# Optimization experiments

Hardware: AMD Instinct MI355X
Metric: run time of the kernel (lower is better)

## Reference

```python
import jax, jax.numpy as jnp
import numpy as np

N_GENE = 4762
N_CELL = 847


def _graph_conv(x_src, src, dst, n_src, n_dst, W, b):
    """DGL GraphConv with norm='both': D_src^{-1/2} A D_dst^{-1/2} X W + b."""
    ones_e = jnp.ones(src.shape, jnp.float32)
    deg_out = jax.ops.segment_sum(ones_e, src, num_segments=n_src)
    norm_src = jnp.clip(deg_out, 1.0, None) ** -0.5
    feat = x_src * norm_src[:, None]            # [n_src, d]
    msg = feat[src]                              # gather  [E, d]
    agg = jax.ops.segment_sum(msg, dst, num_segments=n_dst)  # scatter-add [n_dst, d]
    deg_in = jax.ops.segment_sum(ones_e, dst, num_segments=n_dst)
    norm_dst = jnp.clip(deg_in, 1.0, None) ** -0.5
    return (agg * norm_dst[:, None]) @ W + b


def setup_inputs() -> dict:
    key = jax.random.key(0)
    ks = jax.random.split(key, 12)
    E = 200000
    d = 256
    inp = {
        "gene_emb": jax.random.normal(ks[0], (N_GENE, d), jnp.float32),
        "cell_emb": jax.random.normal(ks[1], (N_CELL, d), jnp.float32),
        "W_g2c": jax.random.normal(ks[2], (d, d), jnp.float32) * (1.0 / np.sqrt(d)),
        "b_g2c": jnp.zeros((d,), jnp.float32),
        "W_c2g": jax.random.normal(ks[3], (d, d), jnp.float32) * (1.0 / np.sqrt(d)),
        "b_c2g": jnp.zeros((d,), jnp.float32),
        "Wp": jax.random.normal(ks[4], (2 * d, 1), jnp.float32) * (1.0 / np.sqrt(2 * d)),
        "bp": jnp.zeros((1,), jnp.float32),
        "g2c_src": jax.random.randint(ks[5], (E,), 0, N_GENE, jnp.int32),
        "g2c_dst": jax.random.randint(ks[6], (E,), 0, N_CELL, jnp.int32),
        "c2g_src": jax.random.randint(ks[7], (E,), 0, N_CELL, jnp.int32),
        "c2g_dst": jax.random.randint(ks[8], (E,), 0, N_GENE, jnp.int32),
        "dec_src": jax.random.randint(ks[9], (E,), 0, N_GENE, jnp.int32),
        "dec_dst": jax.random.randint(ks[10], (E,), 0, N_CELL, jnp.int32),
    }
    return inp


def reference(gene_emb, cell_emb, W_g2c, b_g2c, W_c2g, b_c2g, Wp, bp,
              g2c_src, g2c_dst, c2g_src, c2g_dst, dec_src, dec_dst):
    # HeteroGraphConv (aggregate='sum'): each dst type receives from one relation here.
    h_cell = _graph_conv(gene_emb, g2c_src, g2c_dst, N_GENE, N_CELL, W_g2c, b_g2c)
    h_gene = _graph_conv(cell_emb, c2g_src, c2g_dst, N_CELL, N_GENE, W_c2g, b_c2g)
    h_gene = jax.nn.relu(h_gene)
    h_cell = jax.nn.relu(h_cell)
    # HeteroMLPPredictor: concat(src_h, dst_h) @ Wp + bp on dec_graph edges.
    x = jnp.concatenate([h_gene[dec_src], h_cell[dec_dst]], axis=1)  # [E_dec, 512]
    score = x @ Wp + bp                                               # [E_dec, 1]
    return (score, h_gene, h_cell)
```

## Files before the change

kernel.cpp:

```cpp
#include <hip/hip_runtime.h>

#define N_GENE 4762
#define N_CELL 847
#define NEDGE  200000
#define D      256
#define NPART  64

typedef __attribute__((ext_vector_type(8))) short short8;
typedef __attribute__((ext_vector_type(8))) unsigned short ushort8v;
typedef __attribute__((ext_vector_type(4))) float f32x4;

#define S_G_OUT 0
#define S_C_IN  (S_G_OUT + N_GENE)
#define S_C_OUT (S_C_IN + N_CELL)
#define S_G_IN  (S_C_OUT + N_CELL)
#define NBINS   (S_G_IN + N_GENE)

#define ALIGN8(x) (((x) + 7) & ~7)

#define A_DEG      0
#define A_NRM      (A_DEG + NBINS)
#define A_OFFS_C   (A_NRM + NBINS)
#define A_OFFS_G   (A_OFFS_C + N_CELL + 1)
#define A_SORT_C   ALIGN8(A_OFFS_G + N_GENE + 1)
#define A_SORT_G   (A_SORT_C + 2 * NEDGE)
#define A_PART     (A_SORT_G + 2 * NEDGE)
#define A_SG       (A_PART + NPART * NBINS)
#define A_SC       (A_SG + N_GENE)
#define A_GENE_BF  ALIGN8(A_SC + N_CELL)
#define A_CELL_BF  ALIGN8(A_GENE_BF + N_GENE * D / 2)
#define A_WT1_BF   ALIGN8(A_CELL_BF + N_CELL * D / 2)
#define A_WT2_BF   ALIGN8(A_WT1_BF + D * D / 2)
#define A_AGGC_BF  ALIGN8(A_WT2_BF + D * D / 2)
#define A_AGGG_BF  ALIGN8(A_AGGC_BF + N_CELL * D / 2)

__device__ __forceinline__ unsigned short f2bf(float f) {
    unsigned u = __float_as_uint(f);
    u = (u + 0x7FFFu + ((u >> 16) & 1u)) >> 16;
    return (unsigned short)u;
}
__device__ __forceinline__ float bf2f(unsigned short b) {
    return __uint_as_float(((unsigned)b) << 16);
}

__global__ __launch_bounds__(1024) void k_pre(
        const int* __restrict__ g2c_src, const int* __restrict__ g2c_dst,
        const int* __restrict__ c2g_src, const int* __restrict__ c2g_dst,
        const float* __restrict__ gene_emb, const float* __restrict__ cell_emb,
        const float* __restrict__ W_g2c, const float* __restrict__ W_c2g,
        int* __restrict__ partial,
        unsigned short* __restrict__ gene_bf, unsigned short* __restrict__ cell_bf,
        unsigned short* __restrict__ wt1, unsigned short* __restrict__ wt2) {
    __shared__ int sh[NBINS];
    int B = blockIdx.x, T = threadIdx.x;
    if (B < NPART) {
        for (int j = T; j < NBINS; j += 1024) sh[j] = 0;
        __syncthreads();
        const int chunk = (NEDGE + NPART - 1) / NPART;
        int e0 = B * chunk, e1 = min(NEDGE, e0 + chunk);
        for (int e = e0 + T; e < e1; e += 1024) {
            atomicAdd(&sh[S_G_OUT + g2c_src[e]], 1);
            atomicAdd(&sh[S_C_IN  + g2c_dst[e]], 1);
            atomicAdd(&sh[S_C_OUT + c2g_src[e]], 1);
            atomicAdd(&sh[S_G_IN  + c2g_dst[e]], 1);
        }
        __syncthreads();
        int* pp = partial + B * NBINS;
        for (int j = T; j < NBINS; j += 1024) pp[j] = sh[j];
    } else {
        const int NG = N_GENE * D, NC = N_CELL * D, NW = D * D;
        const int total = NG + NC + 2 * NW;
        for (int i = (B - NPART) * 1024 + T; i < total; i += NPART * 1024) {
            if (i < NG) {
                gene_bf[i] = f2bf(gene_emb[i]);
            } else if (i < NG + NC) {
                int j = i - NG;
                cell_bf[j] = f2bf(cell_emb[j]);
            } else if (i < NG + NC + NW) {
                int j = i - NG - NC;
                wt1[j] = f2bf(W_g2c[(j & 255) * D + (j >> 8)]);
            } else {
                int j = i - NG - NC - NW;
                wt2[j] = f2bf(W_c2g[(j & 255) * D + (j >> 8)]);
            }
        }
    }
}

__global__ void k_reduce(int* __restrict__ partial, int* __restrict__ deg,
                         float* __restrict__ nrm) {
    int j = blockIdx.x * blockDim.x + threadIdx.x;
    if (j < NBINS) {
        int s = 0;
        #pragma unroll
        for (int b0 = 0; b0 < NPART; b0 += 32) {
            int t[32];
            #pragma unroll
            for (int u = 0; u < 32; u++) t[u] = partial[(b0 + u) * NBINS + j];
            #pragma unroll
            for (int u = 0; u < 32; u++) { partial[(b0 + u) * NBINS + j] = s; s += t[u]; }
        }
        deg[j] = s;
        nrm[j] = rsqrtf(fmaxf((float)s, 1.0f));
    }
}

__global__ __launch_bounds__(1024) void k_scatter(
        const int* __restrict__ g2c_src, const int* __restrict__ g2c_dst,
        const int* __restrict__ c2g_src, const int* __restrict__ c2g_dst,
        const int* __restrict__ deg, const int* __restrict__ partial,
        const float* __restrict__ nrm,
        int* __restrict__ offsC, int* __restrict__ offsG,
        int2* __restrict__ sortC, int2* __restrict__ sortG) {
    __shared__ int soffs[N_GENE + 1];
    __shared__ int scur[N_GENE];
    __shared__ int wsum[16];
    int T = threadIdx.x, blk = blockIdx.x, dir = blockIdx.y;
    const int* src  = dir ? c2g_src : g2c_src;
    const int* dst  = dir ? c2g_dst : g2c_dst;
    const int* dgs  = dir ? deg + S_G_IN : deg + S_C_IN;
    const float* nsv = dir ? nrm + S_C_OUT : nrm + S_G_OUT;
    int seg         = dir ? S_G_IN : S_C_IN;
    int nb          = dir ? N_GENE : N_CELL;
    int* goffs      = dir ? offsG : offsC;
    int2* sorted    = dir ? sortG : sortC;
    int per = (nb + 1023) >> 10;
    int i0 = T * per, i1 = min(nb, i0 + per);
    int loc[5];
    int s = 0;
    for (int i = i0; i < i1; i++) { loc[i - i0] = s; s += dgs[i]; }
    int lane = T & 63, w = T >> 6;
    int t = s;
    #pragma unroll
    for (int off = 1; off < 64; off <<= 1) {
        int u = __shfl_up(t, off);
        if (lane >= off) t += u;
    }
    if (lane == 63) wsum[w] = t;
    __syncthreads();
    if (w == 0 && lane < 16) {
        int x = wsum[lane];
        #pragma unroll
        for (int off = 1; off < 16; off <<= 1) {
            int u = __shfl_up(x, off);
            if (lane >= off) x += u;
        }
        wsum[lane] = x;
    }
    __syncthreads();
    int wbase = w ? wsum[w - 1] : 0;
    int excl = wbase + t - s;
    for (int i = i0; i < i1; i++) soffs[i] = excl + loc[i - i0];
    if (T == 1023) soffs[nb] = excl + s;
    __syncthreads();
    if (blk == 0)
        for (int j = T; j <= nb; j += 1024) goffs[j] = soffs[j];
    const int* basep = partial + blk * NBINS + seg;
    for (int j = T; j < nb; j += 1024) scur[j] = soffs[j] + basep[j];
    __syncthreads();
    const int chunk = (NEDGE + NPART - 1) / NPART;
    int e0 = blk * chunk, e1 = min(NEDGE, e0 + chunk);
    for (int e = e0 + T; e < e1; e += 1024) {
        int d = dst[e], sv = src[e];
        float nv = nsv[sv];
        int pos = atomicAdd(&scur[d], 1);
        sorted[pos] = make_int2(sv, __float_as_int(nv));
    }
}

__global__ __launch_bounds__(256) void k_agg(
        const unsigned short* __restrict__ gene_bf,
        const unsigned short* __restrict__ cell_bf,
        const int2* __restrict__ sortC, const int2* __restrict__ sortG,
        const int* __restrict__ offsC, const int* __restrict__ offsG,
        const float* __restrict__ nrm,
        unsigned short* __restrict__ aggC, unsigned short* __restrict__ aggG) {
    __shared__ int   sidx[4][64];
    __shared__ float snrm[4][64];
    __shared__ float pacc[4][256];
    int w = threadIdx.x >> 6, lane = threadIdx.x & 63;
    int half = lane >> 5, li = lane & 31;
    int B = blockIdx.x;
    bool isCell = B < N_CELL;

    int e0, e1;
    const unsigned short* emb;
    const int2* sorted;
    int node;
    if (isCell) {
        node = B;
        int f0 = offsC[node], f1 = offsC[node + 1];
        int ne = f1 - f0, nw = (ne + 3) >> 2;
        e0 = f0 + w * nw; e1 = min(f1, e0 + nw);
        emb = gene_bf; sorted = sortC;
    } else {
        node = (B - N_CELL) * 4 + w;
        if (node >= N_GENE) return;
        e0 = offsG[node]; e1 = offsG[node + 1];
        emb = cell_bf; sorted = sortG;
    }

    float acc[8];
    #pragma unroll
    for (int c = 0; c < 8; c++) acc[c] = 0.f;

    for (int base = e0; base < e1; base += 64) {
        int n = min(64, e1 - base);
        if (lane < n) {
            int2 pr = sorted[base + lane];
            sidx[w][lane] = pr.x;
            snrm[w][lane] = __int_as_float(pr.y);
        }
        int i = 0;
        for (; 2 * i + 8 <= n; i += 4) {
            int j0 = 2 * i + half, j1 = 2 * i + 2 + half;
            int j2 = 2 * i + 4 + half, j3 = 2 * i + 6 + half;
            ushort8v v0 = *(const ushort8v*)&emb[sidx[w][j0] * D + li * 8];
            ushort8v v1 = *(const ushort8v*)&emb[sidx[w][j1] * D + li * 8];
            ushort8v v2 = *(const ushort8v*)&emb[sidx[w][j2] * D + li * 8];
            ushort8v v3 = *(const ushort8v*)&emb[sidx[w][j3] * D + li * 8];
            float n0 = snrm[w][j0], n1 = snrm[w][j1];
            float n2 = snrm[w][j2], n3 = snrm[w][j3];
            #pragma unroll
            for (int c = 0; c < 8; c++)
                acc[c] += bf2f(v0[c]) * n0 + bf2f(v1[c]) * n1 +
                          bf2f(v2[c]) * n2 + bf2f(v3[c]) * n3;
        }
        int npair = (n + 1) >> 1;
        for (; i < npair; i++) {
            int jj = 2 * i + half;
            bool ok = jj < n;
            int idx = ok ? sidx[w][jj] : sidx[w][0];
            float nv = ok ? snrm[w][jj] : 0.f;
            ushort8v v = *(const ushort8v*)&emb[idx * D + li * 8];
            #pragma unroll
            for (int c = 0; c < 8; c++) acc[c] += bf2f(v[c]) * nv;
        }
    }
    #pragma unroll
    for (int c = 0; c < 8; c++) acc[c] += __shfl_xor(acc[c], 32);

    if (isCell) {
        if (half == 0) {
            #pragma unroll
            for (int c = 0; c < 8; c++) pacc[w][li * 8 + c] = acc[c];
        }
        __syncthreads();
        int T = threadIdx.x;
        float s2 = pacc[0][T] + pacc[1][T] + pacc[2][T] + pacc[3][T];
        aggC[node * D + T] = f2bf(s2 * nrm[S_C_IN + node]);
    } else {
        if (half == 0) {
            float ndv = nrm[S_G_IN + node];
            ushort8v o;
            #pragma unroll
            for (int c = 0; c < 8; c++) o[c] = f2bf(acc[c] * ndv);
            *(ushort8v*)&aggG[node * D + li * 8] = o;
        }
    }
}

__global__ __launch_bounds__(256) void k_gemm2(
        const unsigned short* __restrict__ aggC, const unsigned short* __restrict__ aggG,
        const unsigned short* __restrict__ wt1, const unsigned short* __restrict__ wt2,
        const float* __restrict__ b_g2c, const float* __restrict__ b_c2g,
        const float* __restrict__ Wp,
        float* __restrict__ hC, float* __restrict__ hG,
        float* __restrict__ sg, float* __restrict__ sc) {
    const int CT = (N_CELL + 15) / 16;
    const int GT = (N_GENE + 15) / 16;
    int wid = blockIdx.x * 4 + (threadIdx.x >> 6);
    if (wid >= CT + GT) return;
    bool isCell = wid < CT;
    int tile = isCell ? wid : wid - CT;
    int m0 = tile * 16;
    int M = isCell ? N_CELL : N_GENE;
    const unsigned short* A  = isCell ? aggC : aggG;
    const unsigned short* Wt = isCell ? wt1 : wt2;
    const float* bias = isCell ? b_g2c : b_c2g;
    const float* wp   = isCell ? Wp + D : Wp;
    float* H  = isCell ? hC : hG;
    float* sv = isCell ? sc : sg;
    int lane = threadIdx.x & 63;
    int l15 = lane & 15, quad = lane >> 4;
    int arow = m0 + l15;
    if (arow >= M) arow = M - 1;
    f32x4 acc[16];
    #pragma unroll
    for (int t = 0; t < 16; t++) acc[t] = (f32x4){0.f, 0.f, 0.f, 0.f};
    #pragma unroll
    for (int k0 = 0; k0 < D; k0 += 32) {
        short8 a = *(const short8*)&A[arow * D + k0 + quad * 8];
        #pragma unroll
        for (int t = 0; t < 16; t++) {
            short8 b = *(const short8*)&Wt[(t * 16 + l15) * D + k0 + quad * 8];
            acc[t] = __builtin_amdgcn_mfma_f32_16x16x32_bf16(a, b, acc[t], 0, 0, 0);
        }
    }
    float dot[4] = {0.f, 0.f, 0.f, 0.f};
    #pragma unroll
    for (int t = 0; t < 16; t++) {
        int col = t * 16 + l15;
        float bv = bias[col], wv = wp[col];
        #pragma unroll
        for (int r = 0; r < 4; r++) {
            int row = m0 + quad * 4 + r;
            float h = fmaxf(acc[t][r] + bv, 0.f);
            if (row < M) H[row * D + col] = h;
            dot[r] += h * wv;
        }
    }
    #pragma unroll
    for (int off = 1; off < 16; off <<= 1) {
        #pragma unroll
        for (int r = 0; r < 4; r++) dot[r] += __shfl_xor(dot[r], off);
    }
    if (l15 == 0) {
        #pragma unroll
        for (int r = 0; r < 4; r++) {
            int row = m0 + quad * 4 + r;
            if (row < M) sv[row] = dot[r];
        }
    }
}

__global__ void k_score(const int* __restrict__ dsrc, const int* __restrict__ ddst,
                        const float* __restrict__ sg, const float* __restrict__ sc,
                        const float* __restrict__ bp, float* __restrict__ out) {
    int i = blockIdx.x * blockDim.x + threadIdx.x;
    if (i < NEDGE) out[i] = sg[dsrc[i]] + sc[ddst[i]] + bp[0];
}

extern "C" void kernel_launch(void* const* d_in, const int* in_sizes, int n_in,
                              void* d_out, int out_size, void* d_ws, size_t ws_size,
                              hipStream_t stream) {
    const float* gene_emb = (const float*)d_in[0];
    const float* cell_emb = (const float*)d_in[1];
    const float* W_g2c    = (const float*)d_in[2];
    const float* b_g2c    = (const float*)d_in[3];
    const float* W_c2g    = (const float*)d_in[4];
    const float* b_c2g    = (const float*)d_in[5];
    const float* Wp       = (const float*)d_in[6];
    const float* bp       = (const float*)d_in[7];
    const int* g2c_src = (const int*)d_in[8];
    const int* g2c_dst = (const int*)d_in[9];
    const int* c2g_src = (const int*)d_in[10];
    const int* c2g_dst = (const int*)d_in[11];
    const int* dec_src = (const int*)d_in[12];
    const int* dec_dst = (const int*)d_in[13];

    int*   wsi = (int*)d_ws;
    float* wsf = (float*)d_ws;
    unsigned short* gene_bf = (unsigned short*)(wsi + A_GENE_BF);
    unsigned short* cell_bf = (unsigned short*)(wsi + A_CELL_BF);
    unsigned short* wt1     = (unsigned short*)(wsi + A_WT1_BF);
    unsigned short* wt2     = (unsigned short*)(wsi + A_WT2_BF);
    unsigned short* aggC    = (unsigned short*)(wsi + A_AGGC_BF);
    unsigned short* aggG    = (unsigned short*)(wsi + A_AGGG_BF);
    int2* sortC = (int2*)(wsi + A_SORT_C);
    int2* sortG = (int2*)(wsi + A_SORT_G);

    float* out = (float*)d_out;
    float* out_score = out;
    float* out_hgene = out + NEDGE;
    float* out_hcell = out + NEDGE + N_GENE * D;

    k_pre<<<2 * NPART, 1024, 0, stream>>>(g2c_src, g2c_dst, c2g_src, c2g_dst,
                                          gene_emb, cell_emb, W_g2c, W_c2g,
                                          wsi + A_PART, gene_bf, cell_bf, wt1, wt2);
    k_reduce<<<(NBINS + 255) / 256, 256, 0, stream>>>(wsi + A_PART, wsi + A_DEG,
                                                      wsf + A_NRM);
    {
        dim3 grid(NPART, 2);
        k_scatter<<<grid, 1024, 0, stream>>>(g2c_src, g2c_dst, c2g_src, c2g_dst,
                                             wsi + A_DEG, wsi + A_PART, wsf + A_NRM,
                                             wsi + A_OFFS_C, wsi + A_OFFS_G,
                                             sortC, sortG);
    }
    k_agg<<<N_CELL + (N_GENE + 3) / 4, 256, 0, stream>>>(
        gene_bf, cell_bf, sortC, sortG, wsi + A_OFFS_C, wsi + A_OFFS_G,
        wsf + A_NRM, aggC, aggG);
    {
        const int CT = (N_CELL + 15) / 16, GT = (N_GENE + 15) / 16;
        k_gemm2<<<(CT + GT + 3) / 4, 256, 0, stream>>>(aggC, aggG, wt1, wt2,
                                                       b_g2c, b_c2g, Wp,
                                                       out_hcell, out_hgene,
                                                       wsf + A_SG, wsf + A_SC);
    }
    k_score<<<(NEDGE + 255) / 256, 256, 0, stream>>>(dec_src, dec_dst,
                                                     wsf + A_SG, wsf + A_SC, bp, out_score);
}
```

Baseline: 158.9 us.

## Split offset scan into separate kernel, raise edge partitions, unroll gather by eight

Raises the number of edge partitions from 64 to 256 so the histogram and scatter kernels spread across more blocks. The per-block prefix scan moves into a small standalone kernel that runs once per direction, so the scatter blocks no longer repeat it. The scatter kernel also stages the source norms in shared memory instead of reading them from global memory per edge. The aggregation kernel gains an 8-way unrolled gather loop for more memory-level parallelism. In exchange there is one extra kernel launch, the partial-count buffer grows fourfold so the reduce kernel reads more data, and the larger shared-memory use may lower scatter occupancy.

```diff
diff --git a/kernel.cpp b/kernel.cpp
--- a/kernel.cpp
+++ b/kernel.cpp
@@ -4,7 +4,7 @@
 #define N_CELL 847
 #define NEDGE  200000
 #define D      256
-#define NPART  64
+#define NPART  256
 
 typedef __attribute__((ext_vector_type(8))) short short8;
 typedef __attribute__((ext_vector_type(8))) unsigned short ushort8v;
@@ -70,7 +70,7 @@
     } else {
         const int NG = N_GENE * D, NC = N_CELL * D, NW = D * D;
         const int total = NG + NC + 2 * NW;
-        for (int i = (B - NPART) * 1024 + T; i < total; i += NPART * 1024) {
+        for (int i = (B - NPART) * 1024 + T; i < total; i += 64 * 1024) {
             if (i < NG) {
                 gene_bf[i] = f2bf(gene_emb[i]);
             } else if (i < NG + NC) {
@@ -92,7 +92,6 @@
     int j = blockIdx.x * blockDim.x + threadIdx.x;
     if (j < NBINS) {
         int s = 0;
-        #pragma unroll
         for (int b0 = 0; b0 < NPART; b0 += 32) {
             int t[32];
             #pragma unroll
@@ -105,25 +104,14 @@
     }
 }
 
-__global__ __launch_bounds__(1024) void k_scatter(
-        const int* __restrict__ g2c_src, const int* __restrict__ g2c_dst,
-        const int* __restrict__ c2g_src, const int* __restrict__ c2g_dst,
-        const int* __restrict__ deg, const int* __restrict__ partial,
-        const float* __restrict__ nrm,
-        int* __restrict__ offsC, int* __restrict__ offsG,
-        int2* __restrict__ sortC, int2* __restrict__ sortG) {
-    __shared__ int soffs[N_GENE + 1];
-    __shared__ int scur[N_GENE];
+__global__ __launch_bounds__(1024) void k_scan(const int* __restrict__ deg,
+                                               int* __restrict__ offsC,
+                                               int* __restrict__ offsG) {
     __shared__ int wsum[16];
-    int T = threadIdx.x, blk = blockIdx.x, dir = blockIdx.y;
-    const int* src  = dir ? c2g_src : g2c_src;
-    const int* dst  = dir ? c2g_dst : g2c_dst;
-    const int* dgs  = dir ? deg + S_G_IN : deg + S_C_IN;
-    const float* nsv = dir ? nrm + S_C_OUT : nrm + S_G_OUT;
-    int seg         = dir ? S_G_IN : S_C_IN;
-    int nb          = dir ? N_GENE : N_CELL;
-    int* goffs      = dir ? offsG : offsC;
-    int2* sorted    = dir ? sortG : sortC;
+    int dir = blockIdx.x, T = threadIdx.x;
+    const int* dgs = dir ? deg + S_G_IN : deg + S_C_IN;
+    int nb         = dir ? N_GENE : N_CELL;
+    int* goffs     = dir ? offsG : offsC;
     int per = (nb + 1023) >> 10;
     int i0 = T * per, i1 = min(nb, i0 + per);
     int loc[5];
@@ -150,19 +138,38 @@
     __syncthreads();
     int wbase = w ? wsum[w - 1] : 0;
     int excl = wbase + t - s;
-    for (int i = i0; i < i1; i++) soffs[i] = excl + loc[i - i0];
-    if (T == 1023) soffs[nb] = excl + s;
+    for (int i = i0; i < i1; i++) goffs[i] = excl + loc[i - i0];
+    if (T == 1023) goffs[nb] = excl + s;
+}
+
+__global__ __launch_bounds__(1024) void k_scatter(
+        const int* __restrict__ g2c_src, const int* __restrict__ g2c_dst,
+        const int* __restrict__ c2g_src, const int* __restrict__ c2g_dst,
+        const int* __restrict__ partial, const float* __restrict__ nrm,
+        const int* __restrict__ offsC, const int* __restrict__ offsG,
+        int2* __restrict__ sortC, int2* __restrict__ sortG) {
+    __shared__ int   scur[N_GENE];
+    __shared__ float nsrcf[N_GENE];
+    int T = threadIdx.x, blk = blockIdx.x, dir = blockIdx.y;
+    const int* src   = dir ? c2g_src : g2c_src;
+    const int* dst   = dir ? c2g_dst : g2c_dst;
+    int seg          = dir ? S_G_IN : S_C_IN;
+    int sseg         = dir ? S_C_OUT : S_G_OUT;
+    int nb           = dir ? N_GENE : N_CELL;
+    int ns           = dir ? N_CELL : N_GENE;
+    const int* goffs = dir ? offsG : offsC;
+    int2* sorted     = dir ? sortG : sortC;
+
+    for (int j = T; j < ns; j += 1024) nsrcf[j] = nrm[sseg + j];
+    const int* basep = partial + blk * NBINS + seg;
+    for (int j = T; j < nb; j += 1024) scur[j] = goffs[j] + basep[j];
     __syncthreads();
-    if (blk == 0)
-        for (int j = T; j <= nb; j += 1024) goffs[j] = soffs[j];
-    const int* basep = partial + blk * NBINS + seg;
-    for (int j = T; j < nb; j += 1024) scur[j] = soffs[j] + basep[j];
-    __syncthreads();
+
     const int chunk = (NEDGE + NPART - 1) / NPART;
     int e0 = blk * chunk, e1 = min(NEDGE, e0 + chunk);
     for (int e = e0 + T; e < e1; e += 1024) {
         int d = dst[e], sv = src[e];
-        float nv = nsv[sv];
+        float nv = nsrcf[sv];
         int pos = atomicAdd(&scur[d], 1);
         sorted[pos] = make_int2(sv, __float_as_int(nv));
     }
@@ -212,6 +219,23 @@
             snrm[w][lane] = __int_as_float(pr.y);
         }
         int i = 0;
+        for (; 2 * i + 16 <= n; i += 8) {
+            ushort8v v[8];
+            float nv[8];
+            #pragma unroll
+            for (int k = 0; k < 8; k++) {
+                int jj = 2 * i + 2 * k + half;
+                v[k] = *(const ushort8v*)&emb[sidx[w][jj] * D + li * 8];
+                nv[k] = snrm[w][jj];
+            }
+            #pragma unroll
+            for (int c = 0; c < 8; c++) {
+                float s0 = 0.f;
+                #pragma unroll
+                for (int k = 0; k < 8; k++) s0 += bf2f(v[k][c]) * nv[k];
+                acc[c] += s0;
+            }
+        }
         for (; 2 * i + 8 <= n; i += 4) {
             int j0 = 2 * i + half, j1 = 2 * i + 2 + half;
             int j2 = 2 * i + 4 + half, j3 = 2 * i + 6 + half;
@@ -365,15 +389,16 @@
     float* out_hgene = out + NEDGE;
     float* out_hcell = out + NEDGE + N_GENE * D;
 
-    k_pre<<<2 * NPART, 1024, 0, stream>>>(g2c_src, g2c_dst, c2g_src, c2g_dst,
-                                          gene_emb, cell_emb, W_g2c, W_c2g,
-                                          wsi + A_PART, gene_bf, cell_bf, wt1, wt2);
+    k_pre<<<NPART + 64, 1024, 0, stream>>>(g2c_src, g2c_dst, c2g_src, c2g_dst,
+                                           gene_emb, cell_emb, W_g2c, W_c2g,
+                                           wsi + A_PART, gene_bf, cell_bf, wt1, wt2);
     k_reduce<<<(NBINS + 255) / 256, 256, 0, stream>>>(wsi + A_PART, wsi + A_DEG,
                                                       wsf + A_NRM);
+    k_scan<<<2, 1024, 0, stream>>>(wsi + A_DEG, wsi + A_OFFS_C, wsi + A_OFFS_G);
     {
         dim3 grid(NPART, 2);
         k_scatter<<<grid, 1024, 0, stream>>>(g2c_src, g2c_dst, c2g_src, c2g_dst,
-                                             wsi + A_DEG, wsi + A_PART, wsf + A_NRM,
+                                             wsi + A_PART, wsf + A_NRM,
                                              wsi + A_OFFS_C, wsi + A_OFFS_G,
                                              sortC, sortG);
     }
```

Result: slower. 169.9 us (+6.9%).

## Split degree histogram per index array, unroll aggregation by 8, split GEMM over N

Applied to the files above, without the earlier changes.

The degree-count kernel now gives each of the four edge index arrays its own group of 64 blocks, which uses a smaller shared histogram and adds more parallelism. The aggregation loop gains an 8-pair unrolled path so more gather loads are in flight at once. The final GEMM gives each wave a 64-column quarter of the output rather than all 256 columns, so four times as many waves are launched with fewer accumulator registers each. Because each row's score dot product is now split across waves, it is combined with float atomics into buffers zeroed in the prep kernel, which makes the summation order nondeterministic.

```diff
diff --git a/kernel.cpp b/kernel.cpp
--- a/kernel.cpp
+++ b/kernel.cpp
@@ -50,27 +50,30 @@
         const float* __restrict__ W_g2c, const float* __restrict__ W_c2g,
         int* __restrict__ partial,
         unsigned short* __restrict__ gene_bf, unsigned short* __restrict__ cell_bf,
-        unsigned short* __restrict__ wt1, unsigned short* __restrict__ wt2) {
-    __shared__ int sh[NBINS];
+        unsigned short* __restrict__ wt1, unsigned short* __restrict__ wt2,
+        float* __restrict__ sg, float* __restrict__ sc) {
+    __shared__ int sh[N_GENE];
     int B = blockIdx.x, T = threadIdx.x;
-    if (B < NPART) {
-        for (int j = T; j < NBINS; j += 1024) sh[j] = 0;
+    if (B < 4 * NPART) {
+        int grp = B >> 6, blk = B & (NPART - 1);
+        const int* idx;
+        int segbase, segn;
+        if      (grp == 0) { idx = g2c_src; segbase = S_G_OUT; segn = N_GENE; }
+        else if (grp == 1) { idx = g2c_dst; segbase = S_C_IN;  segn = N_CELL; }
+        else if (grp == 2) { idx = c2g_src; segbase = S_C_OUT; segn = N_CELL; }
+        else               { idx = c2g_dst; segbase = S_G_IN;  segn = N_GENE; }
+        for (int j = T; j < segn; j += 1024) sh[j] = 0;
         __syncthreads();
         const int chunk = (NEDGE + NPART - 1) / NPART;
-        int e0 = B * chunk, e1 = min(NEDGE, e0 + chunk);
-        for (int e = e0 + T; e < e1; e += 1024) {
-            atomicAdd(&sh[S_G_OUT + g2c_src[e]], 1);
-            atomicAdd(&sh[S_C_IN  + g2c_dst[e]], 1);
-            atomicAdd(&sh[S_C_OUT + c2g_src[e]], 1);
-            atomicAdd(&sh[S_G_IN  + c2g_dst[e]], 1);
-        }
+        int e0 = blk * chunk, e1 = min(NEDGE, e0 + chunk);
+        for (int e = e0 + T; e < e1; e += 1024) atomicAdd(&sh[idx[e]], 1);
         __syncthreads();
-        int* pp = partial + B * NBINS;
-        for (int j = T; j < NBINS; j += 1024) pp[j] = sh[j];
+        int* pp = partial + blk * NBINS + segbase;
+        for (int j = T; j < segn; j += 1024) pp[j] = sh[j];
     } else {
         const int NG = N_GENE * D, NC = N_CELL * D, NW = D * D;
         const int total = NG + NC + 2 * NW;
-        for (int i = (B - NPART) * 1024 + T; i < total; i += NPART * 1024) {
+        for (int i = (B - 4 * NPART) * 1024 + T; i < total; i += 64 * 1024) {
             if (i < NG) {
                 gene_bf[i] = f2bf(gene_emb[i]);
             } else if (i < NG + NC) {
@@ -83,6 +86,9 @@
                 int j = i - NG - NC - NW;
                 wt2[j] = f2bf(W_c2g[(j & 255) * D + (j >> 8)]);
             }
+        }
+        for (int i = (B - 4 * NPART) * 1024 + T; i < N_GENE + N_CELL; i += 64 * 1024) {
+            if (i < N_GENE) sg[i] = 0.f; else sc[i - N_GENE] = 0.f;
         }
     }
 }
@@ -212,6 +218,23 @@
             snrm[w][lane] = __int_as_float(pr.y);
         }
         int i = 0;
+        for (; 2 * i + 16 <= n; i += 8) {
+            ushort8v v[8];
+            float nv[8];
+            #pragma unroll
+            for (int k = 0; k < 8; k++) {
+                int jj = 2 * i + 2 * k + half;
+                v[k] = *(const ushort8v*)&emb[sidx[w][jj] * D + li * 8];
+                nv[k] = snrm[w][jj];
+            }
+            #pragma unroll
+            for (int c = 0; c < 8; c++) {
+                float s0 = 0.f;
+                #pragma unroll
+                for (int k = 0; k < 8; k++) s0 += bf2f(v[k][c]) * nv[k];
+                acc[c] += s0;
+            }
+        }
         for (; 2 * i + 8 <= n; i += 4) {
             int j0 = 2 * i + half, j1 = 2 * i + 2 + half;
             int j2 = 2 * i + 4 + half, j3 = 2 * i + 6 + half;
@@ -270,9 +293,11 @@
     const int CT = (N_CELL + 15) / 16;
     const int GT = (N_GENE + 15) / 16;
     int wid = blockIdx.x * 4 + (threadIdx.x >> 6);
-    if (wid >= CT + GT) return;
-    bool isCell = wid < CT;
-    int tile = isCell ? wid : wid - CT;
+    if (wid >= (CT + GT) * 4) return;
+    int tid = wid >> 2, nq = wid & 3;
+    int n0 = nq * 64;
+    bool isCell = tid < CT;
+    int tile = isCell ? tid : tid - CT;
     int m0 = tile * 16;
     int M = isCell ? N_CELL : N_GENE;
     const unsigned short* A  = isCell ? aggC : aggG;
@@ -285,22 +310,22 @@
     int l15 = lane & 15, quad = lane >> 4;
     int arow = m0 + l15;
     if (arow >= M) arow = M - 1;
-    f32x4 acc[16];
-    #pragma unroll
-    for (int t = 0; t < 16; t++) acc[t] = (f32x4){0.f, 0.f, 0.f, 0.f};
+    f32x4 acc[4];
+    #pragma unroll
+    for (int t = 0; t < 4; t++) acc[t] = (f32x4){0.f, 0.f, 0.f, 0.f};
     #pragma unroll
     for (int k0 = 0; k0 < D; k0 += 32) {
         short8 a = *(const short8*)&A[arow * D + k0 + quad * 8];
         #pragma unroll
-        for (int t = 0; t < 16; t++) {
-            short8 b = *(const short8*)&Wt[(t * 16 + l15) * D + k0 + quad * 8];
+        for (int t = 0; t < 4; t++) {
+            short8 b = *(const short8*)&Wt[(n0 + t * 16 + l15) * D + k0 + quad * 8];
             acc[t] = __builtin_amdgcn_mfma_f32_16x16x32_bf16(a, b, acc[t], 0, 0, 0);
         }
     }
     float dot[4] = {0.f, 0.f, 0.f, 0.f};
     #pragma unroll
-    for (int t = 0; t < 16; t++) {
-        int col = t * 16 + l15;
+    for (int t = 0; t < 4; t++) {
+        int col = n0 + t * 16 + l15;
         float bv = bias[col], wv = wp[col];
         #pragma unroll
         for (int r = 0; r < 4; r++) {
@@ -319,7 +344,7 @@
         #pragma unroll
         for (int r = 0; r < 4; r++) {
             int row = m0 + quad * 4 + r;
-            if (row < M) sv[row] = dot[r];
+            if (row < M) atomicAdd(&sv[row], dot[r]);
         }
     }
 }
@@ -365,9 +390,10 @@
     float* out_hgene = out + NEDGE;
     float* out_hcell = out + NEDGE + N_GENE * D;
 
-    k_pre<<<2 * NPART, 1024, 0, stream>>>(g2c_src, g2c_dst, c2g_src, c2g_dst,
-                                          gene_emb, cell_emb, W_g2c, W_c2g,
-                                          wsi + A_PART, gene_bf, cell_bf, wt1, wt2);
+    k_pre<<<4 * NPART + 64, 1024, 0, stream>>>(g2c_src, g2c_dst, c2g_src, c2g_dst,
+                                               gene_emb, cell_emb, W_g2c, W_c2g,
+                                               wsi + A_PART, gene_bf, cell_bf, wt1, wt2,
+                                               wsf + A_SG, wsf + A_SC);
     k_reduce<<<(NBINS + 255) / 256, 256, 0, stream>>>(wsi + A_PART, wsi + A_DEG,
                                                       wsf + A_NRM);
     {
@@ -382,10 +408,10 @@
         wsf + A_NRM, aggC, aggG);
     {
         const int CT = (N_CELL + 15) / 16, GT = (N_GENE + 15) / 16;
-        k_gemm2<<<(CT + GT + 3) / 4, 256, 0, stream>>>(aggC, aggG, wt1, wt2,
-                                                       b_g2c, b_c2g, Wp,
-                                                       out_hcell, out_hgene,
-                                                       wsf + A_SG, wsf + A_SC);
+        k_gemm2<<<CT + GT, 256, 0, stream>>>(aggC, aggG, wt1, wt2,
+                                             b_g2c, b_c2g, Wp,
+                                             out_hcell, out_hgene,
+                                             wsf + A_SG, wsf + A_SC);
     }
     k_score<<<(NEDGE + 255) / 256, 256, 0, stream>>>(dec_src, dec_dst,
                                                      wsf + A_SG, wsf + A_SC, bp, out_score);
```

Result: faster. 140.7 us (median of 2 runs) (-11.5%).
